# Performance work log

Hardware: AMD Instinct MI355X
Metric: run time of the kernel (lower is better)

Reference implementation:

```python
import jax, jax.numpy as jnp
import numpy as np

D_MODEL = 1024
NUM_ATOMS = 16384
TEMPERATURE = 1.0
NEG_INF = -1e9


def setup_inputs() -> dict:
    key = jax.random.key(0)
    kx, kd, km = jax.random.split(key, 3)
    x = jax.random.normal(kx, (4, 2048, D_MODEL), dtype=jnp.float32)
    # xavier_uniform for [num_atoms, d_model]
    limit = float(np.sqrt(6.0 / (NUM_ATOMS + D_MODEL)))
    dictionary = jax.random.uniform(
        kd, (NUM_ATOMS, D_MODEL), dtype=jnp.float32, minval=-limit, maxval=limit
    )
    mask = jax.random.randint(km, (4, 2048, NUM_ATOMS), 0, 2, dtype=jnp.int32)
    return {"x": x, "dictionary": dictionary, "mask": mask}


def reference(x, dictionary, mask):
    # scores: [b, s, num_atoms]
    scores = jnp.einsum("bsd,ad->bsa", x, dictionary)
    m = mask.astype(scores.dtype)
    scores = scores * m + (1.0 - m) * NEG_INF
    weights = jax.nn.softmax(scores / TEMPERATURE, axis=-1)
    reconstruction = jnp.einsum("bsa,ad->bsd", weights, dictionary)
    argmax_indices = jnp.argmax(scores, axis=-1)
    return reconstruction, argmax_indices
```

## Files before the change

### kernel.cpp

```cpp
#include <hip/hip_runtime.h>

#define NTOK   8192
#define DMODEL 1024
#define NATOM  16384

typedef _Float16 half8  __attribute__((ext_vector_type(8)));
typedef _Float16 half4_t __attribute__((ext_vector_type(4)));
typedef float    f32x4  __attribute__((ext_vector_type(4)));

#define GLOAD_LDS16(gsrc, ldst) \
  __builtin_amdgcn_global_load_lds((const __attribute__((address_space(1))) unsigned int*)(gsrc), \
                                   (__attribute__((address_space(3))) unsigned int*)(ldst), 16, 0, 0)

__global__ void cvt_f32_f16(const float* __restrict__ in, _Float16* __restrict__ out, int n4) {
  int i = blockIdx.x * 256 + threadIdx.x;
  if (i >= n4) return;
  float4 v = ((const float4*)in)[i];
  half4_t h;
  h[0] = (_Float16)v.x; h[1] = (_Float16)v.y; h[2] = (_Float16)v.z; h[3] = (_Float16)v.w;
  ((half4_t*)out)[i] = h;
}

__global__ void transpose_dict(const float* __restrict__ dict,
                               _Float16* __restrict__ Dh, _Float16* __restrict__ dT) {
  __shared__ _Float16 tile[64][68];
  int a0 = blockIdx.x * 64;
  int d0 = blockIdx.y * 64;
  int tid = threadIdx.x;
  int c = tid & 63;
  int r0 = tid >> 6;
  #pragma unroll
  for (int i = 0; i < 16; i++) {
    int r = r0 + i * 4;
    _Float16 h = (_Float16)dict[(size_t)(a0 + r) * DMODEL + d0 + c];
    tile[r][c] = h;
    Dh[(size_t)(a0 + r) * DMODEL + d0 + c] = h;
  }
  __syncthreads();
  #pragma unroll
  for (int i = 0; i < 16; i++) {
    int rd = r0 + i * 4;
    dT[(size_t)(d0 + rd) * NATOM + a0 + c] = tile[c][rd];
  }
}

__global__ void zero_lsum(float* __restrict__ lsum) {
  lsum[blockIdx.x * 256 + threadIdx.x] = 0.0f;
}

__device__ __forceinline__ void stage_ab(const _Float16* __restrict__ A,
                                         const _Float16* __restrict__ B,
                                         _Float16* As, _Float16* Bs,
                                         size_t arow0, size_t brow0, size_t ldk,
                                         int k0, int tid) {
  #pragma unroll
  for (int i = 0; i < 2; i++) {
    int L = tid + i * 256;
    int r = L >> 2, pc = L & 3;
    int c = pc ^ ((r >> 1) & 3);
    GLOAD_LDS16(A + (arow0 + r) * ldk + k0 + c * 8, As + (size_t)L * 8);
    GLOAD_LDS16(B + (brow0 + r) * ldk + k0 + c * 8, Bs + (size_t)L * 8);
  }
}

__device__ __forceinline__ void stage_item(const _Float16* __restrict__ src, int row0,
                                           int kt, int s, _Float16* dst, int tid) {
  #pragma unroll
  for (int i = 0; i < 2; i++) {
    int L2 = tid + i * 512;
    int r = L2 >> 2, q = L2 & 3;
    int c = s * 4 + (q ^ (r & 3));
    GLOAD_LDS16(src + (size_t)(row0 + r) * DMODEL + kt * 64 + c * 8, dst + (size_t)L2 * 8);
  }
}

__launch_bounds__(512, 2)
__global__ void score_kernel(const _Float16* __restrict__ Xh,
                             const _Float16* __restrict__ Dh,
                             const int* __restrict__ mask,
                             _Float16* __restrict__ E,
                             float* __restrict__ lsum,
                             _Float16* __restrict__ Tmax) {
  __shared__ _Float16 lds[65536];
  const int tid  = threadIdx.x;
  const int lane = tid & 63;
  const int wave = tid >> 6;
  const int wm = wave >> 2;
  const int wn = wave & 3;
  const int m0 = blockIdx.y * 256;
  const int n0 = blockIdx.x * 256;

  const int frow = lane & 15;
  const int fkc  = lane >> 4;

  f32x4 acc[8][4] = {};

  #define AOFF(B_, S_, ROW_) ((B_) * 32768 + (S_) * 8192 + (((ROW_) << 2) + (fkc ^ ((ROW_) & 3))) * 8)
  #define BOFF(B_, S_, ROW_) ((B_) * 32768 + 16384 + (S_) * 8192 + (((ROW_) << 2) + (fkc ^ ((ROW_) & 3))) * 8)

  stage_item(Xh, m0, 0, 0, lds,         tid);
  stage_item(Dh, n0, 0, 0, lds + 16384, tid);
  stage_item(Xh, m0, 0, 1, lds + 8192,  tid);
  stage_item(Dh, n0, 0, 1, lds + 24576, tid);
  asm volatile("s_waitcnt vmcnt(4)" ::: "memory");
  __builtin_amdgcn_s_barrier();

  const int NKT = DMODEL / 64;
  for (int kt = 0; kt < NKT; ++kt) {
    const int b  = kt & 1;
    const int nb = b ^ 1;
    const bool more = (kt + 1 < NKT);
    half8 af[4], bf[4];

    #pragma unroll
    for (int i = 0; i < 4; i++) af[i] = *(const half8*)&lds[AOFF(b, 0, wm * 128 + i * 16 + frow)];
    #pragma unroll
    for (int j = 0; j < 4; j++) bf[j] = *(const half8*)&lds[BOFF(b, 0, wn * 64 + j * 16 + frow)];
    if (more) stage_item(Xh, m0, kt + 1, 0, lds + nb * 32768, tid);
    asm volatile("s_waitcnt lgkmcnt(0)" ::: "memory");
    __builtin_amdgcn_sched_barrier(0);
    __builtin_amdgcn_s_setprio(1);
    #pragma unroll
    for (int i = 0; i < 4; i++)
      #pragma unroll
      for (int j = 0; j < 4; j++)
        acc[i][j] = __builtin_amdgcn_mfma_f32_16x16x32_f16(af[i], bf[j], acc[i][j], 0, 0, 0);
    __builtin_amdgcn_s_setprio(0);
    __builtin_amdgcn_sched_barrier(0);
    __builtin_amdgcn_s_barrier();

    #pragma unroll
    for (int i = 0; i < 4; i++) af[i] = *(const half8*)&lds[AOFF(b, 0, wm * 128 + 64 + i * 16 + frow)];
    if (more) stage_item(Dh, n0, kt + 1, 0, lds + nb * 32768 + 16384, tid);
    asm volatile("s_waitcnt lgkmcnt(0)" ::: "memory");
    __builtin_amdgcn_sched_barrier(0);
    __builtin_amdgcn_s_setprio(1);
    #pragma unroll
    for (int i = 0; i < 4; i++)
      #pragma unroll
      for (int j = 0; j < 4; j++)
        acc[4 + i][j] = __builtin_amdgcn_mfma_f32_16x16x32_f16(af[i], bf[j], acc[4 + i][j], 0, 0, 0);
    __builtin_amdgcn_s_setprio(0);
    __builtin_amdgcn_sched_barrier(0);
    if (more) asm volatile("s_waitcnt vmcnt(4)" ::: "memory");
    else      asm volatile("s_waitcnt vmcnt(0)" ::: "memory");
    __builtin_amdgcn_s_barrier();

    #pragma unroll
    for (int i = 0; i < 4; i++) af[i] = *(const half8*)&lds[AOFF(b, 1, wm * 128 + i * 16 + frow)];
    #pragma unroll
    for (int j = 0; j < 4; j++) bf[j] = *(const half8*)&lds[BOFF(b, 1, wn * 64 + j * 16 + frow)];
    if (more) stage_item(Xh, m0, kt + 1, 1, lds + nb * 32768 + 8192, tid);
    asm volatile("s_waitcnt lgkmcnt(0)" ::: "memory");
    __builtin_amdgcn_sched_barrier(0);
    __builtin_amdgcn_s_setprio(1);
    #pragma unroll
    for (int i = 0; i < 4; i++)
      #pragma unroll
      for (int j = 0; j < 4; j++)
        acc[i][j] = __builtin_amdgcn_mfma_f32_16x16x32_f16(af[i], bf[j], acc[i][j], 0, 0, 0);
    __builtin_amdgcn_s_setprio(0);
    __builtin_amdgcn_sched_barrier(0);
    __builtin_amdgcn_s_barrier();

    #pragma unroll
    for (int i = 0; i < 4; i++) af[i] = *(const half8*)&lds[AOFF(b, 1, wm * 128 + 64 + i * 16 + frow)];
    if (more) stage_item(Dh, n0, kt + 1, 1, lds + nb * 32768 + 24576, tid);
    asm volatile("s_waitcnt lgkmcnt(0)" ::: "memory");
    __builtin_amdgcn_sched_barrier(0);
    __builtin_amdgcn_s_setprio(1);
    #pragma unroll
    for (int i = 0; i < 4; i++)
      #pragma unroll
      for (int j = 0; j < 4; j++)
        acc[4 + i][j] = __builtin_amdgcn_mfma_f32_16x16x32_f16(af[i], bf[j], acc[4 + i][j], 0, 0, 0);
    __builtin_amdgcn_s_setprio(0);
    __builtin_amdgcn_sched_barrier(0);
    if (more) asm volatile("s_waitcnt vmcnt(4)" ::: "memory");
    __builtin_amdgcn_s_barrier();
  }
  #undef AOFF
  #undef BOFF

  const int cr = (lane >> 4) * 4;
  const int cc = lane & 15;
  const int rr = tid >> 1, hh = tid & 1;
  float s_acc = 0.0f;
  #pragma unroll
  for (int h = 0; h < 2; h++) {
    if ((wn >> 1) == h) {
      #pragma unroll
      for (int i = 0; i < 8; i++) {
        #pragma unroll
        for (int j = 0; j < 4; j++) {
          #pragma unroll
          for (int r = 0; r < 4; r++) {
            int lr = wm * 128 + i * 16 + cr + r;
            int lc = (wn & 1) * 64 + j * 16 + cc;
            int mk = mask[(size_t)(m0 + lr) * NATOM + n0 + h * 128 + lc];
            float e = mk ? __expf(acc[i][j][r]) : 0.0f;
            lds[lr * 136 + lc] = (_Float16)e;
          }
        }
      }
    }
    __builtin_amdgcn_s_barrier();
    #pragma unroll
    for (int i = 0; i < 8; i++) {
      int chunk = i * 512 + tid;
      int r  = chunk >> 4;
      int c8 = (chunk & 15) * 8;
      *(half8*)&E[(size_t)(m0 + r) * NATOM + n0 + h * 128 + c8] = *(const half8*)&lds[r * 136 + c8];
    }
    {
      const _Float16* rowp = &lds[rr * 136 + hh * 64];
      float s = 0.0f, m = 0.0f;
      #pragma unroll
      for (int i = 0; i < 8; i++) {
        half8 v = *(const half8*)&rowp[i * 8];
        #pragma unroll
        for (int j = 0; j < 8; j++) { float f = (float)v[j]; s += f; m = fmaxf(m, f); }
      }
      s += __shfl_xor(s, 1, 64);
      m = fmaxf(m, __shfl_xor(m, 1, 64));
      if (hh == 0) {
        s_acc += s;
        Tmax[(size_t)(m0 + rr) * 128 + blockIdx.x * 2 + h] = (_Float16)m;
      }
    }
    __builtin_amdgcn_s_barrier();
  }
  if (hh == 0) atomicAdd(&lsum[m0 + rr], s_acc);
}

__global__ void scan_lite(const _Float16* __restrict__ E,
                          const _Float16* __restrict__ Tmax,
                          const float* __restrict__ x,
                          const float* __restrict__ dict,
                          float* __restrict__ argout) {
  const int wv   = threadIdx.x >> 6;
  const int lane = threadIdx.x & 63;
  const int t = blockIdx.x * 4 + wv;

  __shared__ int    cnt[4];
  __shared__ int    cand[4][32];
  __shared__ double csc[4][32];
  if (lane == 0) cnt[wv] = 0;

  const _Float16* tm = Tmax + (size_t)t * 128;
  float m0 = (float)tm[lane];
  float m1 = (float)tm[64 + lane];
  float mx = fmaxf(m0, m1);
  #pragma unroll
  for (int off = 32; off > 0; off >>= 1) mx = fmaxf(mx, __shfl_xor(mx, off, 64));

  if (mx > 0.0f) {
    float thr = 0.98f * mx;
    unsigned long long q0 = __ballot(m0 >= thr);
    unsigned long long q1 = __ballot(m1 >= thr);
    while (q0 | q1) {
      int tile;
      if (q0) { tile = __ffsll(q0) - 1; q0 &= q0 - 1; }
      else    { tile = 64 + __ffsll(q1) - 1; q1 &= q1 - 1; }
      const _Float16* ep = E + (size_t)t * NATOM + tile * 128;
      float e0 = (float)ep[lane], e1 = (float)ep[64 + lane];
      if (e0 >= thr) { int p = atomicAdd(&cnt[wv], 1); if (p < 32) cand[wv][p] = tile * 128 + lane; }
      if (e1 >= thr) { int p = atomicAdd(&cnt[wv], 1); if (p < 32) cand[wv][p] = tile * 128 + 64 + lane; }
    }
  }
  int nc = min(cnt[wv], 32);
  const float* xr = x + (size_t)t * DMODEL;
  for (int c = 0; c < nc; c++) {
    const float* dr = dict + (size_t)cand[wv][c] * DMODEL;
    double a = 0.0;
    #pragma unroll
    for (int i = 0; i < 16; i++) {
      int d = lane + i * 64;
      a += (double)xr[d] * (double)dr[d];
    }
    #pragma unroll
    for (int off = 32; off > 0; off >>= 1) a += __shfl_down(a, off, 64);
    if (lane == 0) csc[wv][c] = a;
  }
  if (lane == 0) {
    int best = 0;
    if (nc > 0) {
      double bs = -1e300;
      best = NATOM;
      for (int c = 0; c < nc; c++)
        if (csc[wv][c] > bs || (csc[wv][c] == bs && cand[wv][c] < best)) { bs = csc[wv][c]; best = cand[wv][c]; }
    }
    argout[t] = (float)best;
  }
}

__launch_bounds__(256, 2)
__global__ void recon_kernel(const _Float16* __restrict__ E,
                             const _Float16* __restrict__ DT,
                             const float* __restrict__ lsum,
                             float* __restrict__ out) {
  __shared__ _Float16 lds[32768];
  const int tid  = threadIdx.x;
  const int lane = tid & 63;
  const int wave = tid >> 6;
  const int wm = wave >> 1, wn = wave & 1;
  const int swz = (blockIdx.x & 7) * 64 + (blockIdx.x >> 3);
  const int n0 = (swz & 7) * 128;
  const int m0 = (swz >> 3) * 128;

  const int frow = lane & 15;
  const int fkc  = lane >> 4;

  f32x4 acc[4][4] = {};

  stage_ab(E, DT, lds,         lds + 4096,  m0, n0, NATOM, 0,  tid);
  stage_ab(E, DT, lds + 8192,  lds + 12288, m0, n0, NATOM, 32, tid);
  stage_ab(E, DT, lds + 16384, lds + 20480, m0, n0, NATOM, 64, tid);

  for (int t = 0; t < 512; ++t) {
    if (t < 510)       asm volatile("s_waitcnt vmcnt(8)" ::: "memory");
    else if (t == 510) asm volatile("s_waitcnt vmcnt(4)" ::: "memory");
    else               asm volatile("s_waitcnt vmcnt(0)" ::: "memory");
    __builtin_amdgcn_s_barrier();
    __builtin_amdgcn_sched_barrier(0);
    const _Float16* As = lds + (t & 3) * 8192;
    const _Float16* Bs = As + 4096;
    half8 af[4], bf[4];
    #pragma unroll
    for (int i = 0; i < 4; i++) {
      int ar = wm * 64 + i * 16 + frow;
      int br = wn * 64 + i * 16 + frow;
      af[i] = *(const half8*)&As[ar * 32 + ((fkc ^ ((ar >> 1) & 3)) << 3)];
      bf[i] = *(const half8*)&Bs[br * 32 + ((fkc ^ ((br >> 1) & 3)) << 3)];
    }
    if (t + 3 < 512) {
      int b = (t + 3) & 3;
      stage_ab(E, DT, lds + b * 8192, lds + b * 8192 + 4096, m0, n0, NATOM, (t + 3) * 32, tid);
    }
    __builtin_amdgcn_s_setprio(1);
    #pragma unroll
    for (int i = 0; i < 4; i++)
      #pragma unroll
      for (int j = 0; j < 4; j++)
        acc[i][j] = __builtin_amdgcn_mfma_f32_16x16x32_f16(af[i], bf[j], acc[i][j], 0, 0, 0);
    __builtin_amdgcn_s_setprio(0);
    __builtin_amdgcn_sched_barrier(0);
  }

  const int cr = (lane >> 4) * 4;
  const int cc = lane & 15;
  #pragma unroll
  for (int i = 0; i < 4; i++) {
    #pragma unroll
    for (int r = 0; r < 4; r++) {
      int lr = wm * 64 + i * 16 + cr + r;
      float sc = 1.0f / lsum[m0 + lr];
      #pragma unroll
      for (int j = 0; j < 4; j++) {
        int lc = wn * 64 + j * 16 + cc;
        out[(size_t)(m0 + lr) * DMODEL + (n0 + lc)] = acc[i][j][r] * sc;
      }
    }
  }
}

extern "C" void kernel_launch(void* const* d_in, const int* in_sizes, int n_in,
                              void* d_out, int out_size, void* d_ws, size_t ws_size,
                              hipStream_t stream) {
  const float* x    = (const float*)d_in[0];
  const float* dict = (const float*)d_in[1];
  const int*   mask = (const int*)d_in[2];
  float* recon  = (float*)d_out;
  float* argout = recon + (size_t)NTOK * DMODEL;

  char* w = (char*)d_ws;
  _Float16* Xh = (_Float16*)(w);
  _Float16* Dh = (_Float16*)(w + (size_t)16  * 1024 * 1024);
  _Float16* DT = (_Float16*)(w + (size_t)48  * 1024 * 1024);
  _Float16* E  = (_Float16*)(w + (size_t)80  * 1024 * 1024);
  float*  lsum = (float*)  (w + (size_t)336 * 1024 * 1024);
  _Float16* Tmax = (_Float16*)d_out;

  cvt_f32_f16<<<dim3(NTOK * DMODEL / 4 / 256), 256, 0, stream>>>(x, Xh, NTOK * DMODEL / 4);
  transpose_dict<<<dim3(NATOM / 64, DMODEL / 64), 256, 0, stream>>>(dict, Dh, DT);
  zero_lsum<<<dim3(NTOK / 256), 256, 0, stream>>>(lsum);
  score_kernel<<<dim3(NATOM / 256, NTOK / 256), 512, 0, stream>>>(Xh, Dh, mask, E, lsum, Tmax);
  scan_lite<<<dim3(NTOK / 4), 256, 0, stream>>>(E, Tmax, x, dict, argout);
  recon_kernel<<<dim3(512), 256, 0, stream>>>(E, DT, lsum, recon);
}
```

Before: 1.379 ms.

## Apply mask with coalesced vector loads during E store and change LDS swizzle

The mask is now applied after staging exp values in LDS. Each thread reads 8 contiguous mask ints with two int4 loads, aligned to the coalesced E write, replacing scattered per-element scalar mask loads in the MFMA fragment layout. Row sum and max are reduced by 16-lane shuffles, and each row chunk issues its own atomicAdd. The LDS XOR swizzle for the stage_item path switches from row&3 to (row>>1)&3 to cut bank conflicts. The cost is more atomics (one per 128-column chunk per half) and exp computed for masked entries.

```diff
diff --git a/kernel.cpp b/kernel.cpp
--- a/kernel.cpp
+++ b/kernel.cpp
@@ -69,7 +69,7 @@
   for (int i = 0; i < 2; i++) {
     int L2 = tid + i * 512;
     int r = L2 >> 2, q = L2 & 3;
-    int c = s * 4 + (q ^ (r & 3));
+    int c = s * 4 + (q ^ ((r >> 1) & 3));
     GLOAD_LDS16(src + (size_t)(row0 + r) * DMODEL + kt * 64 + c * 8, dst + (size_t)L2 * 8);
   }
 }
@@ -95,8 +95,8 @@
 
   f32x4 acc[8][4] = {};
 
-  #define AOFF(B_, S_, ROW_) ((B_) * 32768 + (S_) * 8192 + (((ROW_) << 2) + (fkc ^ ((ROW_) & 3))) * 8)
-  #define BOFF(B_, S_, ROW_) ((B_) * 32768 + 16384 + (S_) * 8192 + (((ROW_) << 2) + (fkc ^ ((ROW_) & 3))) * 8)
+  #define AOFF(B_, S_, ROW_) ((B_) * 32768 + (S_) * 8192 + (((ROW_) << 2) + (fkc ^ (((ROW_) >> 1) & 3))) * 8)
+  #define BOFF(B_, S_, ROW_) ((B_) * 32768 + 16384 + (S_) * 8192 + (((ROW_) << 2) + (fkc ^ (((ROW_) >> 1) & 3))) * 8)
 
   stage_item(Xh, m0, 0, 0, lds,         tid);
   stage_item(Dh, n0, 0, 0, lds + 16384, tid);
@@ -184,8 +184,6 @@
 
   const int cr = (lane >> 4) * 4;
   const int cc = lane & 15;
-  const int rr = tid >> 1, hh = tid & 1;
-  float s_acc = 0.0f;
   #pragma unroll
   for (int h = 0; h < 2; h++) {
     if ((wn >> 1) == h) {
@@ -197,9 +195,7 @@
           for (int r = 0; r < 4; r++) {
             int lr = wm * 128 + i * 16 + cr + r;
             int lc = (wn & 1) * 64 + j * 16 + cc;
-            int mk = mask[(size_t)(m0 + lr) * NATOM + n0 + h * 128 + lc];
-            float e = mk ? __expf(acc[i][j][r]) : 0.0f;
-            lds[lr * 136 + lc] = (_Float16)e;
+            lds[lr * 136 + lc] = (_Float16)__expf(acc[i][j][r]);
           }
         }
       }
@@ -210,27 +206,34 @@
       int chunk = i * 512 + tid;
       int r  = chunk >> 4;
       int c8 = (chunk & 15) * 8;
-      *(half8*)&E[(size_t)(m0 + r) * NATOM + n0 + h * 128 + c8] = *(const half8*)&lds[r * 136 + c8];
-    }
-    {
-      const _Float16* rowp = &lds[rr * 136 + hh * 64];
+      half8 v = *(const half8*)&lds[r * 136 + c8];
+      const int* mp = &mask[(size_t)(m0 + r) * NATOM + n0 + h * 128 + c8];
+      int4 k0 = *(const int4*)mp;
+      int4 k1 = *(const int4*)(mp + 4);
+      half8 e;
+      e[0] = k0.x ? v[0] : (_Float16)0.0f;
+      e[1] = k0.y ? v[1] : (_Float16)0.0f;
+      e[2] = k0.z ? v[2] : (_Float16)0.0f;
+      e[3] = k0.w ? v[3] : (_Float16)0.0f;
+      e[4] = k1.x ? v[4] : (_Float16)0.0f;
+      e[5] = k1.y ? v[5] : (_Float16)0.0f;
+      e[6] = k1.z ? v[6] : (_Float16)0.0f;
+      e[7] = k1.w ? v[7] : (_Float16)0.0f;
+      *(half8*)&E[(size_t)(m0 + r) * NATOM + n0 + h * 128 + c8] = e;
       float s = 0.0f, m = 0.0f;
       #pragma unroll
-      for (int i = 0; i < 8; i++) {
-        half8 v = *(const half8*)&rowp[i * 8];
-        #pragma unroll
-        for (int j = 0; j < 8; j++) { float f = (float)v[j]; s += f; m = fmaxf(m, f); }
+      for (int j = 0; j < 8; j++) { float f = (float)e[j]; s += f; m = fmaxf(m, f); }
+      s += __shfl_xor(s, 1, 64); m = fmaxf(m, __shfl_xor(m, 1, 64));
+      s += __shfl_xor(s, 2, 64); m = fmaxf(m, __shfl_xor(m, 2, 64));
+      s += __shfl_xor(s, 4, 64); m = fmaxf(m, __shfl_xor(m, 4, 64));
+      s += __shfl_xor(s, 8, 64); m = fmaxf(m, __shfl_xor(m, 8, 64));
+      if ((tid & 15) == 0) {
+        atomicAdd(&lsum[m0 + r], s);
+        Tmax[(size_t)(m0 + r) * 128 + blockIdx.x * 2 + h] = (_Float16)m;
       }
-      s += __shfl_xor(s, 1, 64);
-      m = fmaxf(m, __shfl_xor(m, 1, 64));
-      if (hh == 0) {
-        s_acc += s;
-        Tmax[(size_t)(m0 + rr) * 128 + blockIdx.x * 2 + h] = (_Float16)m;
-      }
-    }
-    __builtin_amdgcn_s_barrier();
-  }
-  if (hh == 0) atomicAdd(&lsum[m0 + rr], s_acc);
+    }
+    __builtin_amdgcn_s_barrier();
+  }
 }
 
 __global__ void scan_lite(const _Float16* __restrict__ E,
```

Result: no change. 1.406 ms (+1.9%).
